# Optimization experiments

Measured on AMD Instinct MI355X. Metric: run time of the kernel, lower is better.

Reference implementation:

```python
import jax, jax.numpy as jnp
import numpy as np

N_NODES = 10000
N_EDGES = 160000
IN_DIM = 512
HID = 256
HEADS = 4
OUT_DIM = 512
NEG_SLOPE = 0.2  # PyG GATConv default


def _glorot(key, shape):
    fan_in, fan_out = shape[0], shape[-1]
    lim = jnp.sqrt(6.0 / (fan_in + fan_out))
    return jax.random.uniform(key, shape, jnp.float32, -lim, lim)


def setup_inputs() -> dict:
    key = jax.random.key(0)
    ks = jax.random.split(key, 16)
    x = jax.random.normal(ks[0], (N_NODES, IN_DIM), jnp.float32)
    edge_index = jax.random.randint(ks[1], (2, N_EDGES), 0, N_NODES, jnp.int64)
    # layer 1: GATConv(512 -> 256, heads=4, concat) -> out 1024
    W1 = _glorot(ks[2], (IN_DIM, HEADS * HID))
    att_src1 = _glorot(ks[3], (HEADS, HID))
    att_dst1 = _glorot(ks[4], (HEADS, HID))
    b1 = jnp.zeros((HEADS * HID,), jnp.float32)
    # layer 2: GATConv(1024 -> 256, heads=4, concat) -> out 1024
    W2 = _glorot(ks[5], (HEADS * HID, HEADS * HID))
    att_src2 = _glorot(ks[6], (HEADS, HID))
    att_dst2 = _glorot(ks[7], (HEADS, HID))
    b2 = jnp.zeros((HEADS * HID,), jnp.float32)
    # final fc: 1024 -> 512
    fcW = _glorot(ks[8], (HEADS * HID, OUT_DIM))
    fcb = jnp.zeros((OUT_DIM,), jnp.float32)
    return dict(x=x, edge_index=edge_index, W1=W1, att_src1=att_src1,
                att_dst1=att_dst1, b1=b1, W2=W2, att_src2=att_src2,
                att_dst2=att_dst2, b2=b2, fcW=fcW, fcb=fcb)


def gat_conv(x, src, dst, W, att_src, att_dst, bias):
    # x: [N, F_in]; src/dst: [E] (self-loops already included)
    N = x.shape[0]
    h = (x @ W).reshape(N, HEADS, HID)                       # [N, H, C]
    a_src = jnp.sum(h * att_src, axis=-1)                    # [N, H]
    a_dst = jnp.sum(h * att_dst, axis=-1)                    # [N, H]
    e = jax.nn.leaky_relu(a_src[src] + a_dst[dst], NEG_SLOPE)  # [E, H]
    # numerically stable segment softmax over destination nodes
    m = jax.ops.segment_max(e, dst, num_segments=N)          # [N, H]
    e = jnp.exp(e - m[dst])
    s = jax.ops.segment_sum(e, dst, num_segments=N)          # [N, H]
    alpha = e / (s[dst] + 1e-16)                             # [E, H]
    msg = alpha[:, :, None] * h[src]                         # [E, H, C]
    out = jax.ops.segment_sum(msg, dst, num_segments=N)      # [N, H, C]
    return out.reshape(N, HEADS * HID) + bias


def reference(x, edge_index, W1, att_src1, att_dst1, b1,
              W2, att_src2, att_dst2, b2, fcW, fcb):
    N = x.shape[0]
    loops = jnp.arange(N, dtype=edge_index.dtype)
    src = jnp.concatenate([edge_index[0], loops])  # PyG add_self_loops=True
    dst = jnp.concatenate([edge_index[1], loops])
    h = gat_conv(x, src, dst, W1, att_src1, att_dst1, b1)
    h = jax.nn.relu(h)  # dropout is identity in eval mode
    h = gat_conv(h, src, dst, W2, att_src2, att_dst2, b2)
    h = jax.nn.relu(h)
    return h @ fcW + fcb
```

## Files before the change

### kernel.cpp

```cpp
#include <hip/hip_runtime.h>
#include <hip/hip_bf16.h>

#define NN 10000
#define NE 160000
#define NET 170000
#define IN_DIM 512
#define D1 1024
#define HEADS 4
#define HID 256
#define OUT_DIM 512
#define NEG_SLOPE 0.2f

typedef __attribute__((ext_vector_type(8))) short bf16x8;
typedef __attribute__((ext_vector_type(4))) float f32x4;

__device__ inline float b2f(unsigned short b) {
    union { unsigned u; float f; } x; x.u = ((unsigned)b) << 16; return x.f;
}
__device__ inline unsigned short f2b(float f) {
    union { float f; unsigned u; } x; x.f = f;
    unsigned u = x.u;
    unsigned r = u + 0x7FFFu + ((u >> 16) & 1u);
    return (unsigned short)(r >> 16);
}
__device__ inline float lrelu(float v) { return v > 0.f ? v : NEG_SLOPE * v; }

__global__ void init_kernel(const int* ei32, int* flag, int* counts, int* cursor) {
    int i = blockIdx.x * blockDim.x + threadIdx.x;
    if (i < NN) { counts[i] = 0; cursor[i] = 0; }
    if (blockIdx.x == 0) {
        __shared__ int nz;
        if (threadIdx.x == 0) nz = 0;
        __syncthreads();
        int acc = 0;
        for (int k = threadIdx.x; k < 500; k += 256) acc |= ei32[2 * k + 1];
        if (acc) atomicOr(&nz, 1);
        __syncthreads();
        if (threadIdx.x == 0) flag[0] = (nz == 0) ? 1 : 0;
    }
}

__device__ inline void load_edge(const void* ei, int f64, int e, int& s, int& d) {
    if (f64) {
        const long long* p = (const long long*)ei;
        s = (int)p[e]; d = (int)p[NE + e];
    } else {
        const int* p = (const int*)ei;
        s = p[e]; d = p[NE + e];
    }
}

__global__ void count_kernel(const void* ei, const int* flag, int* counts) {
    int e = blockIdx.x * blockDim.x + threadIdx.x;
    if (e >= NET) return;
    int s, d;
    if (e < NE) load_edge(ei, *flag, e, s, d);
    else d = e - NE;
    atomicAdd(&counts[d], 1);
}

__global__ __launch_bounds__(256) void scan_kernel(const int* counts, int* indptr) {
    __shared__ int part[256];
    int t = threadIdx.x;
    int base = t * 40;
    int local[40];
    int sum = 0;
#pragma unroll
    for (int k = 0; k < 40; k++) {
        int i = base + k;
        int c = (i < NN) ? counts[i] : 0;
        local[k] = sum;
        sum += c;
    }
    part[t] = sum;
    __syncthreads();
    for (int off = 1; off < 256; off <<= 1) {
        int v = (t >= off) ? part[t - off] : 0;
        __syncthreads();
        part[t] += v;
        __syncthreads();
    }
    int excl = part[t] - sum;
#pragma unroll
    for (int k = 0; k < 40; k++) {
        int i = base + k;
        if (i < NN) indptr[i] = excl + local[k];
    }
    if (t == 255) indptr[NN] = part[255];
}

__global__ void fill_kernel(const void* ei, const int* flag, const int* indptr,
                            int* cursor, int* csr_src) {
    int e = blockIdx.x * blockDim.x + threadIdx.x;
    if (e >= NET) return;
    int s, d;
    if (e < NE) load_edge(ei, *flag, e, s, d);
    else { s = e - NE; d = s; }
    int pos = indptr[d] + atomicAdd(&cursor[d], 1);
    csr_src[pos] = s;
}

__device__ void tpose_tile(const float* __restrict__ in, unsigned short* __restrict__ out,
                           int R, int C, int bx, int by) {
    __shared__ float tile[32][33];
    int tx = threadIdx.x & 31, ty = threadIdx.x >> 5;
    int c = bx * 32 + tx;
#pragma unroll
    for (int r0 = 0; r0 < 32; r0 += 8) {
        int r = by * 32 + ty + r0;
        tile[ty + r0][tx] = in[(size_t)r * C + c];
    }
    __syncthreads();
    int oc = by * 32 + tx;
#pragma unroll
    for (int r0 = 0; r0 < 32; r0 += 8) {
        int orow = bx * 32 + ty + r0;
        out[(size_t)orow * R + oc] = f2b(tile[tx][ty + r0]);
    }
}

#define CVT_NB 5000
#define TP1_NB 512
#define TP2_NB 1024
#define TP3_NB 512
__global__ __launch_bounds__(256) void prep_kernel(
    const float* __restrict__ x, unsigned short* __restrict__ xb,
    const float* __restrict__ W1, unsigned short* __restrict__ W1t,
    const float* __restrict__ W2, unsigned short* __restrict__ W2t,
    const float* __restrict__ fcW, unsigned short* __restrict__ fcWt) {
    int b = blockIdx.x;
    if (b < CVT_NB) {
        int i = b * 256 + threadIdx.x;
        float4 v = reinterpret_cast<const float4*>(x)[i];
        ushort4 o;
        o.x = f2b(v.x); o.y = f2b(v.y); o.z = f2b(v.z); o.w = f2b(v.w);
        reinterpret_cast<ushort4*>(xb)[i] = o;
        return;
    }
    b -= CVT_NB;
    if (b < TP1_NB) { tpose_tile(W1, W1t, IN_DIM, D1, b & 31, b >> 5); return; }
    b -= TP1_NB;
    if (b < TP2_NB) { tpose_tile(W2, W2t, D1, D1, b & 31, b >> 5); return; }
    b -= TP2_NB;
    tpose_tile(fcW, fcWt, D1, OUT_DIM, b & 15, b >> 4);
}

#define BM 128
#define BN 128
#define BK 64
__global__ __launch_bounds__(256) void gemm128(
    const unsigned short* __restrict__ A, const unsigned short* __restrict__ B,
    const float* __restrict__ bias, float* __restrict__ Cf, unsigned short* __restrict__ Cb,
    int M, int N, int K, int NB) {
    __shared__ __align__(16) unsigned short As[BM * BK];
    __shared__ __align__(16) unsigned short Bs[BN * BK];
    int t = threadIdx.x;
    int nwg = gridDim.x;
    int q = nwg >> 3, r = nwg & 7;
    int xcd = blockIdx.x & 7, jj = blockIdx.x >> 3;
    int wg = (xcd < r ? xcd * (q + 1) : r * (q + 1) + (xcd - r) * q) + jj;
    int row0 = (wg / NB) * BM, col0 = (wg % NB) * BN;

    int w = t >> 6, l = t & 63;
    int wr = w >> 1, wc = w & 1;
    f32x4 acc[4][4] = {};

    int srow = w * 8 + (l >> 3);
    int scs = (((l & 7) ^ (l >> 3)) * 8);
    const unsigned short* ap0 = A + (size_t)min(row0 +  0 + srow, M - 1) * K + scs;
    const unsigned short* ap1 = A + (size_t)min(row0 + 32 + srow, M - 1) * K + scs;
    const unsigned short* ap2 = A + (size_t)min(row0 + 64 + srow, M - 1) * K + scs;
    const unsigned short* ap3 = A + (size_t)min(row0 + 96 + srow, M - 1) * K + scs;
    const unsigned short* bp0 = B + (size_t)(col0 +  0 + srow) * K + scs;
    const unsigned short* bp1 = B + (size_t)(col0 + 32 + srow) * K + scs;
    const unsigned short* bp2 = B + (size_t)(col0 + 64 + srow) * K + scs;
    const unsigned short* bp3 = B + (size_t)(col0 + 96 + srow) * K + scs;
    unsigned short* asd0 = As + 0 * 2048 + w * 512;
    unsigned short* asd1 = As + 1 * 2048 + w * 512;
    unsigned short* asd2 = As + 2 * 2048 + w * 512;
    unsigned short* asd3 = As + 3 * 2048 + w * 512;
    unsigned short* bsd0 = Bs + 0 * 2048 + w * 512;
    unsigned short* bsd1 = Bs + 1 * 2048 + w * 512;
    unsigned short* bsd2 = Bs + 2 * 2048 + w * 512;
    unsigned short* bsd3 = Bs + 3 * 2048 + w * 512;

    int rr = l & 15;
    int rb = (rr & 7) << 4;
    int kb0 = (l >> 4) << 4;
    const char* Ab = (const char*)As;
    const char* Bb = (const char*)Bs;

#define GLD(src, dst) __builtin_amdgcn_global_load_lds( \
        (const __attribute__((address_space(1))) void*)(src), \
        (__attribute__((address_space(3))) void*)(dst), 16, 0, 0)

    for (int k0 = 0; k0 < K; k0 += BK) {
        GLD(ap0, asd0); GLD(ap1, asd1); GLD(ap2, asd2); GLD(ap3, asd3);
        GLD(bp0, bsd0); GLD(bp1, bsd1); GLD(bp2, bsd2); GLD(bp3, bsd3);
        ap0 += BK; ap1 += BK; ap2 += BK; ap3 += BK;
        bp0 += BK; bp1 += BK; bp2 += BK; bp3 += BK;
        __syncthreads();

#pragma unroll
        for (int ks = 0; ks < 2; ks++) {
            int kb = ((ks << 6) | kb0) ^ rb;
            bf16x8 af[4], bfv[4];
#pragma unroll
            for (int mi = 0; mi < 4; mi++)
                af[mi] = *reinterpret_cast<const bf16x8*>(
                    Ab + (wr * 64 + mi * 16 + rr) * 128 + kb);
#pragma unroll
            for (int ni = 0; ni < 4; ni++)
                bfv[ni] = *reinterpret_cast<const bf16x8*>(
                    Bb + (wc * 64 + ni * 16 + rr) * 128 + kb);
#pragma unroll
            for (int mi = 0; mi < 4; mi++)
#pragma unroll
                for (int ni = 0; ni < 4; ni++)
                    acc[mi][ni] = __builtin_amdgcn_mfma_f32_16x16x32_bf16(
                        af[mi], bfv[ni], acc[mi][ni], 0, 0, 0);
        }
        __syncthreads();
    }
#undef GLD

    int c_l = l & 15, r_h = (l >> 4) * 4;
#pragma unroll
    for (int mi = 0; mi < 4; mi++)
#pragma unroll
        for (int ni = 0; ni < 4; ni++) {
            int gc = col0 + wc * 64 + ni * 16 + c_l;
#pragma unroll
            for (int j = 0; j < 4; j++) {
                int gr = row0 + wr * 64 + mi * 16 + r_h + j;
                if (gr < M) {
                    float v = acc[mi][ni][j];
                    if (bias) v += bias[gc];
                    if (Cf) Cf[(size_t)gr * N + gc] = v;
                    if (Cb) Cb[(size_t)gr * N + gc] = f2b(v);
                }
            }
        }
}

__global__ __launch_bounds__(256) void att_kernel(const unsigned short* __restrict__ hb,
                                                  const float* __restrict__ att_s,
                                                  const float* __restrict__ att_d,
                                                  float* __restrict__ aS, float* __restrict__ aD) {
    int n = blockIdx.x;
    int t = threadIdx.x;
    int head = t >> 6, lane = t & 63;
    const unsigned short* hrow = hb + (size_t)n * D1 + head * HID + lane * 4;
    ushort4 hv = *reinterpret_cast<const ushort4*>(hrow);
    float4 as = *reinterpret_cast<const float4*>(att_s + head * HID + lane * 4);
    float4 ad = *reinterpret_cast<const float4*>(att_d + head * HID + lane * 4);
    float h0 = b2f(hv.x), h1 = b2f(hv.y), h2 = b2f(hv.z), h3 = b2f(hv.w);
    float ps = h0 * as.x + h1 * as.y + h2 * as.z + h3 * as.w;
    float pd = h0 * ad.x + h1 * ad.y + h2 * ad.z + h3 * ad.w;
#pragma unroll
    for (int off = 32; off; off >>= 1) {
        ps += __shfl_xor(ps, off);
        pd += __shfl_xor(pd, off);
    }
    if (lane == 0) {
        aS[n * HEADS + head] = ps;
        aD[n * HEADS + head] = pd;
    }
}

__global__ __launch_bounds__(256) void agg_kernel(const unsigned short* __restrict__ hb,
                                                  const float* __restrict__ aS,
                                                  const float* __restrict__ aD,
                                                  const int* __restrict__ indptr,
                                                  const int* __restrict__ csr_src,
                                                  const float* __restrict__ bias,
                                                  unsigned short* __restrict__ outb) {
    int i = blockIdx.x;
    int t = threadIdx.x;
    int beg = indptr[i], deg = indptr[i + 1] - beg;
    __shared__ float ssum[HEADS];
    __shared__ float alpha_s[64 * HEADS];
    __shared__ int src_s[64];
    __shared__ float xacc[128 * 8];
    if (t < HEADS) ssum[t] = 0.f;
    float4 adst = *reinterpret_cast<const float4*>(aD + i * HEADS);
    int g = t >> 7, u = t & 127;
    int headu = u >> 5;
    const unsigned short* hp8 = hb + (size_t)u * 8;
    float a0 = 0, a1 = 0, a2 = 0, a3 = 0, a4 = 0, a5 = 0, a6 = 0, a7 = 0;
    __syncthreads();
    for (int c0 = 0; c0 < deg; c0 += 64) {
        int nj = min(64, deg - c0);
        if (t < 64) {
            int s = 0;
            float e0 = 0.f, e1 = 0.f, e2 = 0.f, e3 = 0.f;
            if (t < nj) {
                s = csr_src[beg + c0 + t];
                float4 a = *reinterpret_cast<const float4*>(aS + s * HEADS);
                e0 = __expf(lrelu(a.x + adst.x));
                e1 = __expf(lrelu(a.y + adst.y));
                e2 = __expf(lrelu(a.z + adst.z));
                e3 = __expf(lrelu(a.w + adst.w));
            }
            src_s[t] = s;
            alpha_s[t * 4 + 0] = e0;
            alpha_s[t * 4 + 1] = e1;
            alpha_s[t * 4 + 2] = e2;
            alpha_s[t * 4 + 3] = e3;
            float v0 = e0, v1 = e1, v2 = e2, v3 = e3;
#pragma unroll
            for (int off = 32; off; off >>= 1) {
                v0 += __shfl_xor(v0, off);
                v1 += __shfl_xor(v1, off);
                v2 += __shfl_xor(v2, off);
                v3 += __shfl_xor(v3, off);
            }
            if (t == 0) { ssum[0] += v0; ssum[1] += v1; ssum[2] += v2; ssum[3] += v3; }
        }
        __syncthreads();
        int nG = (nj + 1 - g) >> 1;
        int nGr = (nG + 7) & ~7;
#define LDROW(idx) (*reinterpret_cast<const bf16x8*>(hp8 + (size_t)src_s[idx] * D1))
        if (nGr) {
            bf16x8 p0 = LDROW(g);
            bf16x8 p1 = LDROW(g + 2);
            bf16x8 p2 = LDROW(g + 4);
            bf16x8 p3 = LDROW(g + 6);
            bf16x8 p4 = LDROW(g + 8);
            bf16x8 p5 = LDROW(g + 10);
            bf16x8 p6 = LDROW(g + 12);
            bf16x8 p7 = LDROW(g + 14);
            for (int k = 0; k < nGr; k += 8) {
                int j0 = g + 2 * k;
                float w0 = alpha_s[(j0) * 4 + headu];
                float w1 = alpha_s[(j0 + 2) * 4 + headu];
                float w2 = alpha_s[(j0 + 4) * 4 + headu];
                float w3 = alpha_s[(j0 + 6) * 4 + headu];
                float w4 = alpha_s[(j0 + 8) * 4 + headu];
                float w5 = alpha_s[(j0 + 10) * 4 + headu];
                float w6 = alpha_s[(j0 + 12) * 4 + headu];
                float w7 = alpha_s[(j0 + 14) * 4 + headu];
                bf16x8 c0v = p0, c1v = p1, c2v = p2, c3v = p3;
                bf16x8 c4v = p4, c5v = p5, c6v = p6, c7v = p7;
                int jn = j0 + 16;
                p0 = LDROW(min(jn, 63));
                p1 = LDROW(min(jn + 2, 63));
                p2 = LDROW(min(jn + 4, 63));
                p3 = LDROW(min(jn + 6, 63));
                p4 = LDROW(min(jn + 8, 63));
                p5 = LDROW(min(jn + 10, 63));
                p6 = LDROW(min(jn + 12, 63));
                p7 = LDROW(min(jn + 14, 63));
                a0 += w0 * b2f((unsigned short)c0v[0]) + w1 * b2f((unsigned short)c1v[0])
                    + w2 * b2f((unsigned short)c2v[0]) + w3 * b2f((unsigned short)c3v[0])
                    + w4 * b2f((unsigned short)c4v[0]) + w5 * b2f((unsigned short)c5v[0])
                    + w6 * b2f((unsigned short)c6v[0]) + w7 * b2f((unsigned short)c7v[0]);
                a1 += w0 * b2f((unsigned short)c0v[1]) + w1 * b2f((unsigned short)c1v[1])
                    + w2 * b2f((unsigned short)c2v[1]) + w3 * b2f((unsigned short)c3v[1])
                    + w4 * b2f((unsigned short)c4v[1]) + w5 * b2f((unsigned short)c5v[1])
                    + w6 * b2f((unsigned short)c6v[1]) + w7 * b2f((unsigned short)c7v[1]);
                a2 += w0 * b2f((unsigned short)c0v[2]) + w1 * b2f((unsigned short)c1v[2])
                    + w2 * b2f((unsigned short)c2v[2]) + w3 * b2f((unsigned short)c3v[2])
                    + w4 * b2f((unsigned short)c4v[2]) + w5 * b2f((unsigned short)c5v[2])
                    + w6 * b2f((unsigned short)c6v[2]) + w7 * b2f((unsigned short)c7v[2]);
                a3 += w0 * b2f((unsigned short)c0v[3]) + w1 * b2f((unsigned short)c1v[3])
                    + w2 * b2f((unsigned short)c2v[3]) + w3 * b2f((unsigned short)c3v[3])
                    + w4 * b2f((unsigned short)c4v[3]) + w5 * b2f((unsigned short)c5v[3])
                    + w6 * b2f((unsigned short)c6v[3]) + w7 * b2f((unsigned short)c7v[3]);
                a4 += w0 * b2f((unsigned short)c0v[4]) + w1 * b2f((unsigned short)c1v[4])
                    + w2 * b2f((unsigned short)c2v[4]) + w3 * b2f((unsigned short)c3v[4])
                    + w4 * b2f((unsigned short)c4v[4]) + w5 * b2f((unsigned short)c5v[4])
                    + w6 * b2f((unsigned short)c6v[4]) + w7 * b2f((unsigned short)c7v[4]);
                a5 += w0 * b2f((unsigned short)c0v[5]) + w1 * b2f((unsigned short)c1v[5])
                    + w2 * b2f((unsigned short)c2v[5]) + w3 * b2f((unsigned short)c3v[5])
                    + w4 * b2f((unsigned short)c4v[5]) + w5 * b2f((unsigned short)c5v[5])
                    + w6 * b2f((unsigned short)c6v[5]) + w7 * b2f((unsigned short)c7v[5]);
                a6 += w0 * b2f((unsigned short)c0v[6]) + w1 * b2f((unsigned short)c1v[6])
                    + w2 * b2f((unsigned short)c2v[6]) + w3 * b2f((unsigned short)c3v[6])
                    + w4 * b2f((unsigned short)c4v[6]) + w5 * b2f((unsigned short)c5v[6])
                    + w6 * b2f((unsigned short)c6v[6]) + w7 * b2f((unsigned short)c7v[6]);
                a7 += w0 * b2f((unsigned short)c0v[7]) + w1 * b2f((unsigned short)c1v[7])
                    + w2 * b2f((unsigned short)c2v[7]) + w3 * b2f((unsigned short)c3v[7])
                    + w4 * b2f((unsigned short)c4v[7]) + w5 * b2f((unsigned short)c5v[7])
                    + w6 * b2f((unsigned short)c6v[7]) + w7 * b2f((unsigned short)c7v[7]);
            }
        }
#undef LDROW
        __syncthreads();
    }
    if (g == 1) {
        xacc[u * 8 + 0] = a0; xacc[u * 8 + 1] = a1;
        xacc[u * 8 + 2] = a2; xacc[u * 8 + 3] = a3;
        xacc[u * 8 + 4] = a4; xacc[u * 8 + 5] = a5;
        xacc[u * 8 + 6] = a6; xacc[u * 8 + 7] = a7;
    }
    __syncthreads();
    if (g == 0) {
        float inv = 1.f / (ssum[headu] + 1e-16f);
        const float* bp = bias + u * 8;
        bf16x8 ov;
        ov[0] = (short)f2b(fmaxf((a0 + xacc[u * 8 + 0]) * inv + bp[0], 0.f));
        ov[1] = (short)f2b(fmaxf((a1 + xacc[u * 8 + 1]) * inv + bp[1], 0.f));
        ov[2] = (short)f2b(fmaxf((a2 + xacc[u * 8 + 2]) * inv + bp[2], 0.f));
        ov[3] = (short)f2b(fmaxf((a3 + xacc[u * 8 + 3]) * inv + bp[3], 0.f));
        ov[4] = (short)f2b(fmaxf((a4 + xacc[u * 8 + 4]) * inv + bp[4], 0.f));
        ov[5] = (short)f2b(fmaxf((a5 + xacc[u * 8 + 5]) * inv + bp[5], 0.f));
        ov[6] = (short)f2b(fmaxf((a6 + xacc[u * 8 + 6]) * inv + bp[6], 0.f));
        ov[7] = (short)f2b(fmaxf((a7 + xacc[u * 8 + 7]) * inv + bp[7], 0.f));
        *reinterpret_cast<bf16x8*>(outb + (size_t)i * D1 + u * 8) = ov;
    }
}

extern "C" void kernel_launch(void* const* d_in, const int* in_sizes, int n_in,
                              void* d_out, int out_size, void* d_ws, size_t ws_size,
                              hipStream_t stream) {
    const float* x   = (const float*)d_in[0];
    const void*  ei  = d_in[1];
    const float* W1  = (const float*)d_in[2];
    const float* as1 = (const float*)d_in[3];
    const float* ad1 = (const float*)d_in[4];
    const float* b1  = (const float*)d_in[5];
    const float* W2  = (const float*)d_in[6];
    const float* as2 = (const float*)d_in[7];
    const float* ad2 = (const float*)d_in[8];
    const float* b2  = (const float*)d_in[9];
    const float* fcW = (const float*)d_in[10];
    const float* fcb = (const float*)d_in[11];
    float* out = (float*)d_out;

    char* ws = (char*)d_ws;
    size_t o = 0;
    auto carve = [&](size_t bytes) -> char* {
        char* p = ws + o;
        o = (o + bytes + 255) & ~(size_t)255;
        return p;
    };
    unsigned short* xb   = (unsigned short*)carve((size_t)NN * IN_DIM * 2);
    unsigned short* hb   = (unsigned short*)carve((size_t)NN * D1 * 2);
    unsigned short* x2b  = (unsigned short*)carve((size_t)NN * D1 * 2);
    unsigned short* W1t  = (unsigned short*)carve((size_t)D1 * IN_DIM * 2);
    unsigned short* W2t  = (unsigned short*)carve((size_t)D1 * D1 * 2);
    unsigned short* fcWt = (unsigned short*)carve((size_t)OUT_DIM * D1 * 2);
    float* aS   = (float*)carve((size_t)NN * HEADS * 4);
    float* aD   = (float*)carve((size_t)NN * HEADS * 4);
    int* counts = (int*)carve((size_t)NN * 4);
    int* cursor = (int*)carve((size_t)NN * 4);
    int* indptr = (int*)carve((size_t)(NN + 1) * 4);
    int* csr_src= (int*)carve((size_t)NET * 4);
    int* flag   = (int*)carve(4);
    (void)ws_size; (void)in_sizes; (void)n_in; (void)out_size;

    init_kernel<<<(NN + 255) / 256, 256, 0, stream>>>((const int*)ei, flag, counts, cursor);
    count_kernel<<<(NET + 255) / 256, 256, 0, stream>>>(ei, flag, counts);
    scan_kernel<<<1, 256, 0, stream>>>(counts, indptr);
    fill_kernel<<<(NET + 255) / 256, 256, 0, stream>>>(ei, flag, indptr, cursor, csr_src);

    prep_kernel<<<CVT_NB + TP1_NB + TP2_NB + TP3_NB, 256, 0, stream>>>(
        x, xb, W1, W1t, W2, W2t, fcW, fcWt);

    const int MB = (NN + BM - 1) / BM;
    gemm128<<<MB * (D1 / BN), 256, 0, stream>>>(xb, W1t, nullptr, nullptr, hb,
                                                NN, D1, IN_DIM, D1 / BN);
    att_kernel<<<NN, 256, 0, stream>>>(hb, as1, ad1, aS, aD);
    agg_kernel<<<NN, 256, 0, stream>>>(hb, aS, aD, indptr, csr_src, b1, x2b);
    gemm128<<<MB * (D1 / BN), 256, 0, stream>>>(x2b, W2t, nullptr, nullptr, hb,
                                                NN, D1, D1, D1 / BN);
    att_kernel<<<NN, 256, 0, stream>>>(hb, as2, ad2, aS, aD);
    agg_kernel<<<NN, 256, 0, stream>>>(hb, aS, aD, indptr, csr_src, b2, x2b);
    gemm128<<<MB * (OUT_DIM / BN), 256, 0, stream>>>(x2b, fcWt, fcb, out, nullptr,
                                                     NN, OUT_DIM, D1, OUT_DIM / BN);
}
```

Before: 275.5 us.

## Map one wavefront per node in attention and aggregation kernels

```diff
diff --git a/kernel.cpp b/kernel.cpp
--- a/kernel.cpp
+++ b/kernel.cpp
@@ -247,24 +247,30 @@
                                                   const float* __restrict__ att_s,
                                                   const float* __restrict__ att_d,
                                                   float* __restrict__ aS, float* __restrict__ aD) {
-    int n = blockIdx.x;
-    int t = threadIdx.x;
-    int head = t >> 6, lane = t & 63;
-    const unsigned short* hrow = hb + (size_t)n * D1 + head * HID + lane * 4;
-    ushort4 hv = *reinterpret_cast<const ushort4*>(hrow);
-    float4 as = *reinterpret_cast<const float4*>(att_s + head * HID + lane * 4);
-    float4 ad = *reinterpret_cast<const float4*>(att_d + head * HID + lane * 4);
-    float h0 = b2f(hv.x), h1 = b2f(hv.y), h2 = b2f(hv.z), h3 = b2f(hv.w);
-    float ps = h0 * as.x + h1 * as.y + h2 * as.z + h3 * as.w;
-    float pd = h0 * ad.x + h1 * ad.y + h2 * ad.z + h3 * ad.w;
-#pragma unroll
-    for (int off = 32; off; off >>= 1) {
+    int node = blockIdx.x * 4 + (threadIdx.x >> 6);
+    int l = threadIdx.x & 63;
+    int head = l >> 4, qq = l & 15;
+    const unsigned short* hrow = hb + (size_t)node * D1 + head * HID + qq * 16;
+    bf16x8 h0 = *reinterpret_cast<const bf16x8*>(hrow);
+    bf16x8 h1 = *reinterpret_cast<const bf16x8*>(hrow + 8);
+    const float* asp = att_s + head * HID + qq * 16;
+    const float* adp = att_d + head * HID + qq * 16;
+    float ps = 0.f, pd = 0.f;
+#pragma unroll
+    for (int c = 0; c < 8; c++) {
+        float hv = b2f((unsigned short)h0[c]);
+        float hw = b2f((unsigned short)h1[c]);
+        ps += hv * asp[c] + hw * asp[8 + c];
+        pd += hv * adp[c] + hw * adp[8 + c];
+    }
+#pragma unroll
+    for (int off = 1; off <= 8; off <<= 1) {
         ps += __shfl_xor(ps, off);
         pd += __shfl_xor(pd, off);
     }
-    if (lane == 0) {
-        aS[n * HEADS + head] = ps;
-        aD[n * HEADS + head] = pd;
+    if (qq == 0) {
+        aS[node * HEADS + head] = ps;
+        aD[node * HEADS + head] = pd;
     }
 }
 
@@ -275,140 +281,58 @@
                                                   const int* __restrict__ csr_src,
                                                   const float* __restrict__ bias,
                                                   unsigned short* __restrict__ outb) {
-    int i = blockIdx.x;
-    int t = threadIdx.x;
-    int beg = indptr[i], deg = indptr[i + 1] - beg;
-    __shared__ float ssum[HEADS];
-    __shared__ float alpha_s[64 * HEADS];
-    __shared__ int src_s[64];
-    __shared__ float xacc[128 * 8];
-    if (t < HEADS) ssum[t] = 0.f;
-    float4 adst = *reinterpret_cast<const float4*>(aD + i * HEADS);
-    int g = t >> 7, u = t & 127;
-    int headu = u >> 5;
-    const unsigned short* hp8 = hb + (size_t)u * 8;
-    float a0 = 0, a1 = 0, a2 = 0, a3 = 0, a4 = 0, a5 = 0, a6 = 0, a7 = 0;
-    __syncthreads();
-    for (int c0 = 0; c0 < deg; c0 += 64) {
-        int nj = min(64, deg - c0);
-        if (t < 64) {
-            int s = 0;
-            float e0 = 0.f, e1 = 0.f, e2 = 0.f, e3 = 0.f;
-            if (t < nj) {
-                s = csr_src[beg + c0 + t];
-                float4 a = *reinterpret_cast<const float4*>(aS + s * HEADS);
-                e0 = __expf(lrelu(a.x + adst.x));
-                e1 = __expf(lrelu(a.y + adst.y));
-                e2 = __expf(lrelu(a.z + adst.z));
-                e3 = __expf(lrelu(a.w + adst.w));
-            }
-            src_s[t] = s;
-            alpha_s[t * 4 + 0] = e0;
-            alpha_s[t * 4 + 1] = e1;
-            alpha_s[t * 4 + 2] = e2;
-            alpha_s[t * 4 + 3] = e3;
-            float v0 = e0, v1 = e1, v2 = e2, v3 = e3;
-#pragma unroll
-            for (int off = 32; off; off >>= 1) {
-                v0 += __shfl_xor(v0, off);
-                v1 += __shfl_xor(v1, off);
-                v2 += __shfl_xor(v2, off);
-                v3 += __shfl_xor(v3, off);
-            }
-            if (t == 0) { ssum[0] += v0; ssum[1] += v1; ssum[2] += v2; ssum[3] += v3; }
+    int node = blockIdx.x * 4 + (threadIdx.x >> 6);
+    int l = threadIdx.x & 63;
+    int head = l >> 4;
+    int beg = indptr[node];
+    int deg = indptr[node + 1] - beg;
+    float adst = aD[node * HEADS + head];
+    const unsigned short* hp = hb + (size_t)l * 16;
+    const int* cs = csr_src + beg;
+    float acc[16];
+#pragma unroll
+    for (int c = 0; c < 16; c++) acc[c] = 0.f;
+    float esum = 0.f;
+    int dm = deg - 1;
+    for (int j = 0; j < deg; j += 4) {
+        int i0 = j, i1 = min(j + 1, dm), i2 = min(j + 2, dm), i3 = min(j + 3, dm);
+        int s0 = cs[i0], s1 = cs[i1], s2 = cs[i2], s3 = cs[i3];
+        const unsigned short* r0 = hp + (size_t)s0 * D1;
+        const unsigned short* r1 = hp + (size_t)s1 * D1;
+        const unsigned short* r2 = hp + (size_t)s2 * D1;
+        const unsigned short* r3 = hp + (size_t)s3 * D1;
+        bf16x8 r0a = *reinterpret_cast<const bf16x8*>(r0);
+        bf16x8 r0b = *reinterpret_cast<const bf16x8*>(r0 + 8);
+        bf16x8 r1a = *reinterpret_cast<const bf16x8*>(r1);
+        bf16x8 r1b = *reinterpret_cast<const bf16x8*>(r1 + 8);
+        bf16x8 r2a = *reinterpret_cast<const bf16x8*>(r2);
+        bf16x8 r2b = *reinterpret_cast<const bf16x8*>(r2 + 8);
+        bf16x8 r3a = *reinterpret_cast<const bf16x8*>(r3);
+        bf16x8 r3b = *reinterpret_cast<const bf16x8*>(r3 + 8);
+        float e0 = __expf(lrelu(aS[s0 * HEADS + head] + adst));
+        float e1 = (j + 1 <= dm) ? __expf(lrelu(aS[s1 * HEADS + head] + adst)) : 0.f;
+        float e2 = (j + 2 <= dm) ? __expf(lrelu(aS[s2 * HEADS + head] + adst)) : 0.f;
+        float e3 = (j + 3 <= dm) ? __expf(lrelu(aS[s3 * HEADS + head] + adst)) : 0.f;
+        esum += e0 + e1 + e2 + e3;
+#pragma unroll
+        for (int c = 0; c < 8; c++) {
+            acc[c] += e0 * b2f((unsigned short)r0a[c]) + e1 * b2f((unsigned short)r1a[c])
+                    + e2 * b2f((unsigned short)r2a[c]) + e3 * b2f((unsigned short)r3a[c]);
+            acc[8 + c] += e0 * b2f((unsigned short)r0b[c]) + e1 * b2f((unsigned short)r1b[c])
+                        + e2 * b2f((unsigned short)r2b[c]) + e3 * b2f((unsigned short)r3b[c]);
         }
-        __syncthreads();
-        int nG = (nj + 1 - g) >> 1;
-        int nGr = (nG + 7) & ~7;
-#define LDROW(idx) (*reinterpret_cast<const bf16x8*>(hp8 + (size_t)src_s[idx] * D1))
-        if (nGr) {
-            bf16x8 p0 = LDROW(g);
-            bf16x8 p1 = LDROW(g + 2);
-            bf16x8 p2 = LDROW(g + 4);
-            bf16x8 p3 = LDROW(g + 6);
-            bf16x8 p4 = LDROW(g + 8);
-            bf16x8 p5 = LDROW(g + 10);
-            bf16x8 p6 = LDROW(g + 12);
-            bf16x8 p7 = LDROW(g + 14);
-            for (int k = 0; k < nGr; k += 8) {
-                int j0 = g + 2 * k;
-                float w0 = alpha_s[(j0) * 4 + headu];
-                float w1 = alpha_s[(j0 + 2) * 4 + headu];
-                float w2 = alpha_s[(j0 + 4) * 4 + headu];
-                float w3 = alpha_s[(j0 + 6) * 4 + headu];
-                float w4 = alpha_s[(j0 + 8) * 4 + headu];
-                float w5 = alpha_s[(j0 + 10) * 4 + headu];
-                float w6 = alpha_s[(j0 + 12) * 4 + headu];
-                float w7 = alpha_s[(j0 + 14) * 4 + headu];
-                bf16x8 c0v = p0, c1v = p1, c2v = p2, c3v = p3;
-                bf16x8 c4v = p4, c5v = p5, c6v = p6, c7v = p7;
-                int jn = j0 + 16;
-                p0 = LDROW(min(jn, 63));
-                p1 = LDROW(min(jn + 2, 63));
-                p2 = LDROW(min(jn + 4, 63));
-                p3 = LDROW(min(jn + 6, 63));
-                p4 = LDROW(min(jn + 8, 63));
-                p5 = LDROW(min(jn + 10, 63));
-                p6 = LDROW(min(jn + 12, 63));
-                p7 = LDROW(min(jn + 14, 63));
-                a0 += w0 * b2f((unsigned short)c0v[0]) + w1 * b2f((unsigned short)c1v[0])
-                    + w2 * b2f((unsigned short)c2v[0]) + w3 * b2f((unsigned short)c3v[0])
-                    + w4 * b2f((unsigned short)c4v[0]) + w5 * b2f((unsigned short)c5v[0])
-                    + w6 * b2f((unsigned short)c6v[0]) + w7 * b2f((unsigned short)c7v[0]);
-                a1 += w0 * b2f((unsigned short)c0v[1]) + w1 * b2f((unsigned short)c1v[1])
-                    + w2 * b2f((unsigned short)c2v[1]) + w3 * b2f((unsigned short)c3v[1])
-                    + w4 * b2f((unsigned short)c4v[1]) + w5 * b2f((unsigned short)c5v[1])
-                    + w6 * b2f((unsigned short)c6v[1]) + w7 * b2f((unsigned short)c7v[1]);
-                a2 += w0 * b2f((unsigned short)c0v[2]) + w1 * b2f((unsigned short)c1v[2])
-                    + w2 * b2f((unsigned short)c2v[2]) + w3 * b2f((unsigned short)c3v[2])
-                    + w4 * b2f((unsigned short)c4v[2]) + w5 * b2f((unsigned short)c5v[2])
-                    + w6 * b2f((unsigned short)c6v[2]) + w7 * b2f((unsigned short)c7v[2]);
-                a3 += w0 * b2f((unsigned short)c0v[3]) + w1 * b2f((unsigned short)c1v[3])
-                    + w2 * b2f((unsigned short)c2v[3]) + w3 * b2f((unsigned short)c3v[3])
-                    + w4 * b2f((unsigned short)c4v[3]) + w5 * b2f((unsigned short)c5v[3])
-                    + w6 * b2f((unsigned short)c6v[3]) + w7 * b2f((unsigned short)c7v[3]);
-                a4 += w0 * b2f((unsigned short)c0v[4]) + w1 * b2f((unsigned short)c1v[4])
-                    + w2 * b2f((unsigned short)c2v[4]) + w3 * b2f((unsigned short)c3v[4])
-                    + w4 * b2f((unsigned short)c4v[4]) + w5 * b2f((unsigned short)c5v[4])
-                    + w6 * b2f((unsigned short)c6v[4]) + w7 * b2f((unsigned short)c7v[4]);
-                a5 += w0 * b2f((unsigned short)c0v[5]) + w1 * b2f((unsigned short)c1v[5])
-                    + w2 * b2f((unsigned short)c2v[5]) + w3 * b2f((unsigned short)c3v[5])
-                    + w4 * b2f((unsigned short)c4v[5]) + w5 * b2f((unsigned short)c5v[5])
-                    + w6 * b2f((unsigned short)c6v[5]) + w7 * b2f((unsigned short)c7v[5]);
-                a6 += w0 * b2f((unsigned short)c0v[6]) + w1 * b2f((unsigned short)c1v[6])
-                    + w2 * b2f((unsigned short)c2v[6]) + w3 * b2f((unsigned short)c3v[6])
-                    + w4 * b2f((unsigned short)c4v[6]) + w5 * b2f((unsigned short)c5v[6])
-                    + w6 * b2f((unsigned short)c6v[6]) + w7 * b2f((unsigned short)c7v[6]);
-                a7 += w0 * b2f((unsigned short)c0v[7]) + w1 * b2f((unsigned short)c1v[7])
-                    + w2 * b2f((unsigned short)c2v[7]) + w3 * b2f((unsigned short)c3v[7])
-                    + w4 * b2f((unsigned short)c4v[7]) + w5 * b2f((unsigned short)c5v[7])
-                    + w6 * b2f((unsigned short)c6v[7]) + w7 * b2f((unsigned short)c7v[7]);
-            }
-        }
-#undef LDROW
-        __syncthreads();
-    }
-    if (g == 1) {
-        xacc[u * 8 + 0] = a0; xacc[u * 8 + 1] = a1;
-        xacc[u * 8 + 2] = a2; xacc[u * 8 + 3] = a3;
-        xacc[u * 8 + 4] = a4; xacc[u * 8 + 5] = a5;
-        xacc[u * 8 + 6] = a6; xacc[u * 8 + 7] = a7;
-    }
-    __syncthreads();
-    if (g == 0) {
-        float inv = 1.f / (ssum[headu] + 1e-16f);
-        const float* bp = bias + u * 8;
-        bf16x8 ov;
-        ov[0] = (short)f2b(fmaxf((a0 + xacc[u * 8 + 0]) * inv + bp[0], 0.f));
-        ov[1] = (short)f2b(fmaxf((a1 + xacc[u * 8 + 1]) * inv + bp[1], 0.f));
-        ov[2] = (short)f2b(fmaxf((a2 + xacc[u * 8 + 2]) * inv + bp[2], 0.f));
-        ov[3] = (short)f2b(fmaxf((a3 + xacc[u * 8 + 3]) * inv + bp[3], 0.f));
-        ov[4] = (short)f2b(fmaxf((a4 + xacc[u * 8 + 4]) * inv + bp[4], 0.f));
-        ov[5] = (short)f2b(fmaxf((a5 + xacc[u * 8 + 5]) * inv + bp[5], 0.f));
-        ov[6] = (short)f2b(fmaxf((a6 + xacc[u * 8 + 6]) * inv + bp[6], 0.f));
-        ov[7] = (short)f2b(fmaxf((a7 + xacc[u * 8 + 7]) * inv + bp[7], 0.f));
-        *reinterpret_cast<bf16x8*>(outb + (size_t)i * D1 + u * 8) = ov;
-    }
+    }
+    float inv = 1.f / (esum + 1e-16f);
+    const float* bp = bias + l * 16;
+    bf16x8 o0, o1;
+#pragma unroll
+    for (int c = 0; c < 8; c++) {
+        o0[c] = (short)f2b(fmaxf(acc[c] * inv + bp[c], 0.f));
+        o1[c] = (short)f2b(fmaxf(acc[8 + c] * inv + bp[8 + c], 0.f));
+    }
+    unsigned short* op = outb + (size_t)node * D1 + l * 16;
+    *reinterpret_cast<bf16x8*>(op) = o0;
+    *reinterpret_cast<bf16x8*>(op + 8) = o1;
 }
 
 extern "C" void kernel_launch(void* const* d_in, const int* in_sizes, int n_in,
@@ -461,12 +385,12 @@
     const int MB = (NN + BM - 1) / BM;
     gemm128<<<MB * (D1 / BN), 256, 0, stream>>>(xb, W1t, nullptr, nullptr, hb,
                                                 NN, D1, IN_DIM, D1 / BN);
-    att_kernel<<<NN, 256, 0, stream>>>(hb, as1, ad1, aS, aD);
-    agg_kernel<<<NN, 256, 0, stream>>>(hb, aS, aD, indptr, csr_src, b1, x2b);
+    att_kernel<<<NN / 4, 256, 0, stream>>>(hb, as1, ad1, aS, aD);
+    agg_kernel<<<NN / 4, 256, 0, stream>>>(hb, aS, aD, indptr, csr_src, b1, x2b);
     gemm128<<<MB * (D1 / BN), 256, 0, stream>>>(x2b, W2t, nullptr, nullptr, hb,
                                                 NN, D1, D1, D1 / BN);
-    att_kernel<<<NN, 256, 0, stream>>>(hb, as2, ad2, aS, aD);
-    agg_kernel<<<NN, 256, 0, stream>>>(hb, aS, aD, indptr, csr_src, b2, x2b);
+    att_kernel<<<NN / 4, 256, 0, stream>>>(hb, as2, ad2, aS, aD);
+    agg_kernel<<<NN / 4, 256, 0, stream>>>(hb, aS, aD, indptr, csr_src, b2, x2b);
     gemm128<<<MB * (OUT_DIM / BN), 256, 0, stream>>>(x2b, fcWt, fcb, out, nullptr,
                                                      NN, OUT_DIM, D1, OUT_DIM / BN);
 }
```

Result: faster. 269.2 us (-2.3%).
